# Kernel optimization log

Measured on AMD Instinct MI355X. Metric: run time of the kernel, lower is better.

The kernel has to match this reference:

```python
import jax, jax.numpy as jnp
import numpy as np

B, C, H, W = 4, 512, 64, 64
D = C // 8  # inter_channels = 64


def setup_inputs() -> dict:
    key = jax.random.key(0)
    ks = jax.random.split(key, 10)
    s = 1.0 / np.sqrt(C)
    so = 1.0 / np.sqrt(D)
    return {
        "x": jax.random.normal(ks[0], (B, C, H, W), dtype=jnp.float32),
        "Wq": jax.random.normal(ks[1], (D, C), dtype=jnp.float32) * s,
        "bq": jnp.zeros((D,), dtype=jnp.float32),
        "Wk": jax.random.normal(ks[2], (D, C), dtype=jnp.float32) * s,
        "bk": jnp.zeros((D,), dtype=jnp.float32),
        "Wv": jax.random.normal(ks[3], (D, C), dtype=jnp.float32) * s,
        "bv": jnp.zeros((D,), dtype=jnp.float32),
        "Wo": jax.random.normal(ks[4], (C, D), dtype=jnp.float32) * so,
        "bo": jnp.zeros((C,), dtype=jnp.float32),
        "gamma": jnp.zeros((1,), dtype=jnp.float32),
    }


def reference(x, Wq, bq, Wk, bk, Wv, bv, Wo, bo, gamma):
    b, c, h, w = x.shape
    n = h * w
    xf = x.reshape(b, c, n)  # (B, C, N)
    # 1x1 convs == channel-mixing matmuls
    q = jnp.einsum("dc,bcn->bnd", Wq, xf) + bq              # (B, N, D)
    k = jnp.einsum("dc,bcn->bdn", Wk, xf) + bk[:, None]      # (B, D, N)
    v = jnp.einsum("dc,bcn->bnd", Wv, xf) + bv               # (B, N, D)
    scores = jnp.einsum("bnd,bdm->bnm", q, k)                # (B, N, N)
    weights = jax.nn.softmax(scores, axis=-1)
    attended = jnp.einsum("bnm,bmd->bnd", weights, v)        # (B, N, D)
    out = jnp.einsum("cd,bnd->bcn", Wo, attended) + bo[:, None]
    out = out.reshape(b, c, h, w)
    return gamma[0] * out + x
```

## Files before the change

### kernel.cpp

```cpp
#include <hip/hip_runtime.h>

#define NB 4
#define CH 512
#define NN 4096
#define DD 64

typedef __attribute__((ext_vector_type(8))) short bf16x8;
typedef __attribute__((ext_vector_type(4))) float f32x4;

#define MFMA(a, b, c) __builtin_amdgcn_mfma_f32_16x16x32_bf16((a), (b), (c), 0, 0, 0)

__device__ inline unsigned short f2bf(float f) {
    unsigned int u = __builtin_bit_cast(unsigned int, f);
    unsigned int r = u + 0x7fffu + ((u >> 16) & 1u);
    return (unsigned short)(r >> 16);
}

__device__ inline unsigned short f2bf_trunc(float f) {
    return (unsigned short)(__builtin_bit_cast(unsigned int, f) >> 16);
}

__device__ inline float bf2f(unsigned short u) {
    return __builtin_bit_cast(float, ((unsigned int)u) << 16);
}

__device__ inline bf16x8 ld8(const unsigned short* p) {
    return *reinterpret_cast<const bf16x8*>(p);
}

__global__ __launch_bounds__(256) void convert_w(
    const float* __restrict__ Wq, const float* __restrict__ Wk,
    const float* __restrict__ Wv, const float* __restrict__ Wo,
    unsigned short* __restrict__ oq, unsigned short* __restrict__ ok,
    unsigned short* __restrict__ ov, unsigned short* __restrict__ oo) {
    int i = blockIdx.x * 256 + threadIdx.x;
    oq[i] = f2bf(Wq[i]);
    ok[i] = f2bf(Wk[i]);
    ov[i] = f2bf(Wv[i]);
    oo[i] = f2bf(Wo[i]);
}

__global__ __launch_bounds__(256) void qkv_kernel(
    const float* __restrict__ x,
    const unsigned short* __restrict__ Wq, const unsigned short* __restrict__ Wk,
    const unsigned short* __restrict__ Wv,
    const float* __restrict__ bq, const float* __restrict__ bk, const float* __restrict__ bv,
    unsigned short* __restrict__ Q, unsigned short* __restrict__ K,
    unsigned short* __restrict__ VT) {
    const int b = blockIdx.x >> 8;
    const int n0 = (blockIdx.x & 255) * 16;
    const int t = threadIdx.x;
    const int lane = t & 63, w = t >> 6;
    const int l15 = lane & 15, g = lane >> 4;

    __shared__ char smraw[49152];
    unsigned short (*sxT)[520] = (unsigned short(*)[520])smraw;
    float (*red)[4][64][12] = (float(*)[4][64][12])smraw;

    {
        const int cbase = t >> 2;
        const int nq = (t & 3) * 4;
#pragma unroll
        for (int p = 0; p < 8; ++p) {
            int c = p * 64 + cbase;
            float4 v = *reinterpret_cast<const float4*>(
                &x[((size_t)(b * CH + c)) * NN + n0 + nq]);
            sxT[nq + 0][c] = f2bf(v.x);
            sxT[nq + 1][c] = f2bf(v.y);
            sxT[nq + 2][c] = f2bf(v.z);
            sxT[nq + 3][c] = f2bf(v.w);
        }
    }
    __syncthreads();

    f32x4 accQ[4], accK[4], accV[4];
    const f32x4 z = {0.f, 0.f, 0.f, 0.f};
#pragma unroll
    for (int i = 0; i < 4; ++i) { accQ[i] = z; accK[i] = z; accV[i] = z; }

    const int wc = w * 128;
#pragma unroll
    for (int i = 0; i < 4; ++i) {
        int c = wc + i * 32 + 8 * g;
        bf16x8 ax = ld8(&sxT[l15][c]);
#pragma unroll
        for (int dt = 0; dt < 4; ++dt) {
            int d = dt * 16 + l15;
            accQ[dt] = MFMA(ax, ld8(&Wq[d * CH + c]), accQ[dt]);
            accK[dt] = MFMA(ax, ld8(&Wk[d * CH + c]), accK[dt]);
            accV[dt] = MFMA(ld8(&Wv[d * CH + c]), ax, accV[dt]);
        }
    }
    __syncthreads();

#pragma unroll
    for (int dt = 0; dt < 4; ++dt) {
        float* dst = &red[dt][w][lane][0];
        *reinterpret_cast<f32x4*>(dst + 0) = accQ[dt];
        *reinterpret_cast<f32x4*>(dst + 4) = accK[dt];
        *reinterpret_cast<f32x4*>(dst + 8) = accV[dt];
    }
    __syncthreads();

    f32x4 q = *reinterpret_cast<const f32x4*>(&red[w][0][lane][0]);
    f32x4 k = *reinterpret_cast<const f32x4*>(&red[w][0][lane][4]);
    f32x4 v = *reinterpret_cast<const f32x4*>(&red[w][0][lane][8]);
#pragma unroll
    for (int src = 1; src < 4; ++src) {
        const float* sp = &red[w][src][lane][0];
        q += *reinterpret_cast<const f32x4*>(sp + 0);
        k += *reinterpret_cast<const f32x4*>(sp + 4);
        v += *reinterpret_cast<const f32x4*>(sp + 8);
    }
    {
        int d = w * 16 + l15;
        float biasq = bq[d], biask = bk[d];
#pragma unroll
        for (int r = 0; r < 4; ++r) {
            int n = n0 + 4 * g + r;
            Q[((size_t)b * NN + n) * DD + d] = f2bf(q[r] + biasq);
            K[((size_t)b * NN + n) * DD + d] = f2bf(k[r] + biask);
        }
#pragma unroll
        for (int r = 0; r < 4; ++r) {
            int dv = w * 16 + 4 * g + r;
            VT[((size_t)b * DD + dv) * NN + n0 + l15] = f2bf(v[r] + bv[dv]);
        }
    }
}

__global__ __launch_bounds__(256) void attn_kernel(
    const unsigned short* __restrict__ Q, const unsigned short* __restrict__ K,
    const unsigned short* __restrict__ VT,
    unsigned short* __restrict__ PO, float* __restrict__ PML, int KVLEN) {
    const int s = blockIdx.x >> 8;
    const int bq_ = blockIdx.x & 255;
    const int b = bq_ >> 6;
    const int n0 = (bq_ & 63) * 64;
    const int t = threadIdx.x;
    const int lane = t & 63, w = t >> 6;
    const int l15 = lane & 15, g = lane >> 4;

    __shared__ unsigned short sK[64][72];
    __shared__ unsigned short sVT[64][72];
    __shared__ unsigned short sP[4][16][76];

    const int qrow = n0 + 16 * w + l15;
    bf16x8 qf0 = ld8(&Q[((size_t)b * NN + qrow) * DD + 0 + 8 * g]);
    bf16x8 qf1 = ld8(&Q[((size_t)b * NN + qrow) * DD + 32 + 8 * g]);

    f32x4 oacc[4];
    const f32x4 z = {0.f, 0.f, 0.f, 0.f};
#pragma unroll
    for (int i = 0; i < 4; ++i) oacc[i] = z;
    float m_run[4], l_part[4];
#pragma unroll
    for (int r = 0; r < 4; ++r) { m_run[r] = -1e30f; l_part[r] = 0.f; }

    const int kv_begin = s * KVLEN;
    const int kv_end = kv_begin + KVLEN;
    const int srow = t >> 2, sc16 = (t & 3) * 16;

    bf16x8 pk0, pk1, pv0, pv1;
    {
        const unsigned short* kp = &K[((size_t)b * NN + kv_begin + srow) * DD + sc16];
        pk0 = ld8(kp); pk1 = ld8(kp + 8);
        const unsigned short* vp = &VT[((size_t)b * DD + srow) * NN + kv_begin + sc16];
        pv0 = ld8(vp); pv1 = ld8(vp + 8);
    }

    for (int m0 = kv_begin; m0 < kv_end; m0 += 64) {
        *reinterpret_cast<bf16x8*>(&sK[srow][sc16]) = pk0;
        *reinterpret_cast<bf16x8*>(&sK[srow][sc16 + 8]) = pk1;
        *reinterpret_cast<bf16x8*>(&sVT[srow][sc16]) = pv0;
        *reinterpret_cast<bf16x8*>(&sVT[srow][sc16 + 8]) = pv1;
        __syncthreads();

        if (m0 + 64 < kv_end) {
            const unsigned short* kp = &K[((size_t)b * NN + m0 + 64 + srow) * DD + sc16];
            pk0 = ld8(kp); pk1 = ld8(kp + 8);
            const unsigned short* vp = &VT[((size_t)b * DD + srow) * NN + m0 + 64 + sc16];
            pv0 = ld8(vp); pv1 = ld8(vp + 8);
        }

        f32x4 sv[4];
#pragma unroll
        for (int ct = 0; ct < 4; ++ct) sv[ct] = z;
#pragma unroll
        for (int ct = 0; ct < 4; ++ct) {
            bf16x8 kf0 = ld8(&sK[ct * 16 + l15][0 + 8 * g]);
            sv[ct] = MFMA(qf0, kf0, sv[ct]);
            bf16x8 kf1 = ld8(&sK[ct * 16 + l15][32 + 8 * g]);
            sv[ct] = MFMA(qf1, kf1, sv[ct]);
        }

        float ownmax[4];
        bool ok = true;
#pragma unroll
        for (int r = 0; r < 4; ++r) {
            ownmax[r] = fmaxf(fmaxf(sv[0][r], sv[1][r]), fmaxf(sv[2][r], sv[3][r]));
            ok = ok && (ownmax[r] <= m_run[r] + 8.f);
        }
        if (!__all(ok)) {
#pragma unroll
            for (int r = 0; r < 4; ++r) {
                float mx = ownmax[r];
#pragma unroll
                for (int d_ = 8; d_ >= 1; d_ >>= 1) mx = fmaxf(mx, __shfl_xor(mx, d_, 64));
                float mnew = fmaxf(m_run[r], mx);
                float c_ = __expf(m_run[r] - mnew);
                m_run[r] = mnew;
                l_part[r] *= c_;
#pragma unroll
                for (int dt = 0; dt < 4; ++dt) oacc[dt][r] *= c_;
            }
        }
#pragma unroll
        for (int r = 0; r < 4; ++r) {
            float p0 = __expf(sv[0][r] - m_run[r]);
            float p1 = __expf(sv[1][r] - m_run[r]);
            float p2 = __expf(sv[2][r] - m_run[r]);
            float p3 = __expf(sv[3][r] - m_run[r]);
            sv[0][r] = p0; sv[1][r] = p1; sv[2][r] = p2; sv[3][r] = p3;
            l_part[r] += (p0 + p1) + (p2 + p3);
        }

#pragma unroll
        for (int ct = 0; ct < 4; ++ct)
#pragma unroll
            for (int r = 0; r < 4; ++r)
                sP[w][4 * g + r][ct * 16 + l15] = f2bf_trunc(sv[ct][r]);

#pragma unroll
        for (int kk = 0; kk < 2; ++kk) {
            bf16x8 pf = ld8(&sP[w][l15][kk * 32 + 8 * g]);
#pragma unroll
            for (int dt = 0; dt < 4; ++dt) {
                bf16x8 vf = ld8(&sVT[dt * 16 + l15][kk * 32 + 8 * g]);
                oacc[dt] = MFMA(pf, vf, oacc[dt]);
            }
        }
        __syncthreads();
    }

#pragma unroll
    for (int r = 0; r < 4; ++r) {
        float lt = l_part[r];
#pragma unroll
        for (int d_ = 8; d_ >= 1; d_ >>= 1) lt += __shfl_xor(lt, d_, 64);
        int n = n0 + 16 * w + 4 * g + r;
        size_t rowidx = (size_t)s * NB * NN + (size_t)b * NN + n;
#pragma unroll
        for (int dt = 0; dt < 4; ++dt)
            PO[rowidx * DD + dt * 16 + l15] = f2bf(oacc[dt][r]);
        if (l15 == 0) {
            PML[rowidx * 2 + 0] = m_run[r];
            PML[rowidx * 2 + 1] = lt;
        }
    }
}

__global__ __launch_bounds__(256) void out_fused(
    const unsigned short* __restrict__ Wo, const unsigned short* __restrict__ PO,
    const float* __restrict__ PML, const float* __restrict__ bo,
    const float* __restrict__ gamma, const float* __restrict__ x,
    float* __restrict__ out, int S) {
    const int bid = blockIdx.x;
    const int b = bid >> 8;
    const int rest = bid & 255;
    const int n0 = (rest >> 2) * 64;
    const int c0 = (rest & 3) * 128;
    const int t = threadIdx.x;
    const int lane = t & 63, w = t >> 6;
    const int l15 = lane & 15, g = lane >> 4;

    __shared__ unsigned short sATT[64][72];

    {
        const int row = t >> 2;
        const int dq = (t & 3) * 16;
        const size_t base = (size_t)b * NN + n0 + row;
        float m = -1e30f;
        for (int s = 0; s < S; ++s)
            m = fmaxf(m, PML[((size_t)s * NB * NN + base) * 2]);
        float acc[16];
#pragma unroll
        for (int j = 0; j < 16; ++j) acc[j] = 0.f;
        float l = 0.f;
        for (int s = 0; s < S; ++s) {
            size_t rowidx = (size_t)s * NB * NN + base;
            float ms = PML[rowidx * 2 + 0];
            float ls = PML[rowidx * 2 + 1];
            float wgt = __expf(ms - m);
            l += wgt * ls;
            bf16x8 a0 = ld8(&PO[rowidx * DD + dq]);
            bf16x8 a1 = ld8(&PO[rowidx * DD + dq + 8]);
#pragma unroll
            for (int j = 0; j < 8; ++j) {
                acc[j] += wgt * bf2f((unsigned short)a0[j]);
                acc[8 + j] += wgt * bf2f((unsigned short)a1[j]);
            }
        }
        float inv = 1.f / l;
        bf16x8 o0, o1;
#pragma unroll
        for (int j = 0; j < 8; ++j) {
            o0[j] = (short)f2bf(acc[j] * inv);
            o1[j] = (short)f2bf(acc[8 + j] * inv);
        }
        *reinterpret_cast<bf16x8*>(&sATT[row][dq]) = o0;
        *reinterpret_cast<bf16x8*>(&sATT[row][dq + 8]) = o1;
    }
    __syncthreads();

    const int cw = c0 + w * 32;
    f32x4 acc2[2][4];
    const f32x4 z = {0.f, 0.f, 0.f, 0.f};
#pragma unroll
    for (int i = 0; i < 2; ++i)
#pragma unroll
        for (int j = 0; j < 4; ++j) acc2[i][j] = z;

#pragma unroll
    for (int kk = 0; kk < 2; ++kk) {
        bf16x8 af[2], bfr[4];
#pragma unroll
        for (int ct = 0; ct < 2; ++ct)
            af[ct] = ld8(&Wo[(cw + ct * 16 + l15) * DD + kk * 32 + 8 * g]);
#pragma unroll
        for (int nt = 0; nt < 4; ++nt)
            bfr[nt] = ld8(&sATT[nt * 16 + l15][kk * 32 + 8 * g]);
#pragma unroll
        for (int ct = 0; ct < 2; ++ct)
#pragma unroll
            for (int nt = 0; nt < 4; ++nt) acc2[ct][nt] = MFMA(af[ct], bfr[nt], acc2[ct][nt]);
    }

    float gm = gamma[0];
#pragma unroll
    for (int ct = 0; ct < 2; ++ct) {
        int c = cw + ct * 16 + 4 * g;
#pragma unroll
        for (int r = 0; r < 4; ++r) {
            float bias = bo[c + r];
#pragma unroll
            for (int nt = 0; nt < 4; ++nt) {
                int n = n0 + nt * 16 + l15;
                size_t idx = ((size_t)b * CH + c + r) * NN + n;
                out[idx] = gm * (acc2[ct][nt][r] + bias) + x[idx];
            }
        }
    }
}

extern "C" void kernel_launch(void* const* d_in, const int* in_sizes, int n_in,
                              void* d_out, int out_size, void* d_ws, size_t ws_size,
                              hipStream_t stream) {
    const float* x = (const float*)d_in[0];
    const float* Wq = (const float*)d_in[1];
    const float* bq = (const float*)d_in[2];
    const float* Wk = (const float*)d_in[3];
    const float* bk = (const float*)d_in[4];
    const float* Wv = (const float*)d_in[5];
    const float* bv = (const float*)d_in[6];
    const float* Wo = (const float*)d_in[7];
    const float* bo = (const float*)d_in[8];
    const float* gamma = (const float*)d_in[9];
    float* out = (float*)d_out;

    char* ws = (char*)d_ws;
    unsigned short* Wq_bf = (unsigned short*)(ws + 0);
    unsigned short* Wk_bf = (unsigned short*)(ws + 65536);
    unsigned short* Wv_bf = (unsigned short*)(ws + 131072);
    unsigned short* Wo_bf = (unsigned short*)(ws + 196608);
    unsigned short* Qb = (unsigned short*)(ws + 262144);
    unsigned short* Kb = (unsigned short*)(ws + 262144 + 2097152);
    unsigned short* VTb = (unsigned short*)(ws + 262144 + 2 * 2097152);
    const size_t po_off = 262144 + 3ull * 2097152;

    int S = 4;
    while (S > 1 &&
           ws_size < po_off + (size_t)S * (2097152ull + 131072ull))
        S >>= 1;
    unsigned short* PO = (unsigned short*)(ws + po_off);
    float* PML = (float*)(ws + po_off + (size_t)S * 2097152ull);

    hipLaunchKernelGGL(convert_w, dim3(128), dim3(256), 0, stream,
                       Wq, Wk, Wv, Wo, Wq_bf, Wk_bf, Wv_bf, Wo_bf);
    hipLaunchKernelGGL(qkv_kernel, dim3(1024), dim3(256), 0, stream,
                       x, Wq_bf, Wk_bf, Wv_bf, bq, bk, bv, Qb, Kb, VTb);
    hipLaunchKernelGGL(attn_kernel, dim3(256 * S), dim3(256), 0, stream,
                       Qb, Kb, VTb, PO, PML, NN / S);
    hipLaunchKernelGGL(out_fused, dim3(1024), dim3(256), 0, stream,
                       Wo_bf, PO, PML, bo, gamma, x, out, S);
}
```

Baseline: 195.6 us.

## Drop LDS staging in attention, use exp2 softmax, remove QKV cross-wave reduction

Attention now loads K and V^T fragments directly from global memory instead of staging tiles in shared memory, removing the per-tile barriers and the register prefetch. Q is prescaled by log2(e) so all softmax exponentials use the native exp2 instruction. The QKV projection is reorganised so each wave owns 16 output dims across all channels, eliminating the shared-memory reduction and its syncs. Direct global loads rely on cache hits, risk poor coalescing especially for the strided V^T reads, and lose the overlap the prefetch gave.

```diff
diff --git a/kernel.cpp b/kernel.cpp
--- a/kernel.cpp
+++ b/kernel.cpp
@@ -4,6 +4,7 @@
 #define CH 512
 #define NN 4096
 #define DD 64
+#define LOG2E 1.44269504088896f
 
 typedef __attribute__((ext_vector_type(8))) short bf16x8;
 typedef __attribute__((ext_vector_type(4))) float f32x4;
@@ -53,9 +54,7 @@
     const int lane = t & 63, w = t >> 6;
     const int l15 = lane & 15, g = lane >> 4;
 
-    __shared__ char smraw[49152];
-    unsigned short (*sxT)[520] = (unsigned short(*)[520])smraw;
-    float (*red)[4][64][12] = (float(*)[4][64][12])smraw;
+    __shared__ unsigned short sxT[16][520];
 
     {
         const int cbase = t >> 2;
@@ -73,58 +72,29 @@
     }
     __syncthreads();
 
-    f32x4 accQ[4], accK[4], accV[4];
-    const f32x4 z = {0.f, 0.f, 0.f, 0.f};
-#pragma unroll
-    for (int i = 0; i < 4; ++i) { accQ[i] = z; accK[i] = z; accV[i] = z; }
-
-    const int wc = w * 128;
-#pragma unroll
-    for (int i = 0; i < 4; ++i) {
-        int c = wc + i * 32 + 8 * g;
+    const int d = w * 16 + l15;
+    f32x4 aQ = {0.f, 0.f, 0.f, 0.f}, aK = aQ, aV = aQ;
+#pragma unroll
+    for (int i = 0; i < 16; ++i) {
+        int c = i * 32 + 8 * g;
         bf16x8 ax = ld8(&sxT[l15][c]);
-#pragma unroll
-        for (int dt = 0; dt < 4; ++dt) {
-            int d = dt * 16 + l15;
-            accQ[dt] = MFMA(ax, ld8(&Wq[d * CH + c]), accQ[dt]);
-            accK[dt] = MFMA(ax, ld8(&Wk[d * CH + c]), accK[dt]);
-            accV[dt] = MFMA(ld8(&Wv[d * CH + c]), ax, accV[dt]);
-        }
-    }
-    __syncthreads();
-
-#pragma unroll
-    for (int dt = 0; dt < 4; ++dt) {
-        float* dst = &red[dt][w][lane][0];
-        *reinterpret_cast<f32x4*>(dst + 0) = accQ[dt];
-        *reinterpret_cast<f32x4*>(dst + 4) = accK[dt];
-        *reinterpret_cast<f32x4*>(dst + 8) = accV[dt];
-    }
-    __syncthreads();
-
-    f32x4 q = *reinterpret_cast<const f32x4*>(&red[w][0][lane][0]);
-    f32x4 k = *reinterpret_cast<const f32x4*>(&red[w][0][lane][4]);
-    f32x4 v = *reinterpret_cast<const f32x4*>(&red[w][0][lane][8]);
-#pragma unroll
-    for (int src = 1; src < 4; ++src) {
-        const float* sp = &red[w][src][lane][0];
-        q += *reinterpret_cast<const f32x4*>(sp + 0);
-        k += *reinterpret_cast<const f32x4*>(sp + 4);
-        v += *reinterpret_cast<const f32x4*>(sp + 8);
-    }
+        aQ = MFMA(ax, ld8(&Wq[d * CH + c]), aQ);
+        aK = MFMA(ax, ld8(&Wk[d * CH + c]), aK);
+        aV = MFMA(ld8(&Wv[d * CH + c]), ax, aV);
+    }
+
     {
-        int d = w * 16 + l15;
         float biasq = bq[d], biask = bk[d];
 #pragma unroll
         for (int r = 0; r < 4; ++r) {
             int n = n0 + 4 * g + r;
-            Q[((size_t)b * NN + n) * DD + d] = f2bf(q[r] + biasq);
-            K[((size_t)b * NN + n) * DD + d] = f2bf(k[r] + biask);
+            Q[((size_t)b * NN + n) * DD + d] = f2bf((aQ[r] + biasq) * LOG2E);
+            K[((size_t)b * NN + n) * DD + d] = f2bf(aK[r] + biask);
         }
 #pragma unroll
         for (int r = 0; r < 4; ++r) {
             int dv = w * 16 + 4 * g + r;
-            VT[((size_t)b * DD + dv) * NN + n0 + l15] = f2bf(v[r] + bv[dv]);
+            VT[((size_t)b * DD + dv) * NN + n0 + l15] = f2bf(aV[r] + bv[dv]);
         }
     }
 }
@@ -141,8 +111,6 @@
     const int lane = t & 63, w = t >> 6;
     const int l15 = lane & 15, g = lane >> 4;
 
-    __shared__ unsigned short sK[64][72];
-    __shared__ unsigned short sVT[64][72];
     __shared__ unsigned short sP[4][16][76];
 
     const int qrow = n0 + 16 * w + l15;
@@ -159,38 +127,19 @@
 
     const int kv_begin = s * KVLEN;
     const int kv_end = kv_begin + KVLEN;
-    const int srow = t >> 2, sc16 = (t & 3) * 16;
-
-    bf16x8 pk0, pk1, pv0, pv1;
-    {
-        const unsigned short* kp = &K[((size_t)b * NN + kv_begin + srow) * DD + sc16];
-        pk0 = ld8(kp); pk1 = ld8(kp + 8);
-        const unsigned short* vp = &VT[((size_t)b * DD + srow) * NN + kv_begin + sc16];
-        pv0 = ld8(vp); pv1 = ld8(vp + 8);
-    }
 
     for (int m0 = kv_begin; m0 < kv_end; m0 += 64) {
-        *reinterpret_cast<bf16x8*>(&sK[srow][sc16]) = pk0;
-        *reinterpret_cast<bf16x8*>(&sK[srow][sc16 + 8]) = pk1;
-        *reinterpret_cast<bf16x8*>(&sVT[srow][sc16]) = pv0;
-        *reinterpret_cast<bf16x8*>(&sVT[srow][sc16 + 8]) = pv1;
-        __syncthreads();
-
-        if (m0 + 64 < kv_end) {
-            const unsigned short* kp = &K[((size_t)b * NN + m0 + 64 + srow) * DD + sc16];
-            pk0 = ld8(kp); pk1 = ld8(kp + 8);
-            const unsigned short* vp = &VT[((size_t)b * DD + srow) * NN + m0 + 64 + sc16];
-            pv0 = ld8(vp); pv1 = ld8(vp + 8);
-        }
+        const unsigned short* Kb_ = &K[((size_t)b * NN + m0) * DD];
+        const unsigned short* Vb_ = &VT[(size_t)b * DD * NN + m0];
 
         f32x4 sv[4];
 #pragma unroll
         for (int ct = 0; ct < 4; ++ct) sv[ct] = z;
 #pragma unroll
         for (int ct = 0; ct < 4; ++ct) {
-            bf16x8 kf0 = ld8(&sK[ct * 16 + l15][0 + 8 * g]);
+            bf16x8 kf0 = ld8(&Kb_[(ct * 16 + l15) * DD + 0 + 8 * g]);
             sv[ct] = MFMA(qf0, kf0, sv[ct]);
-            bf16x8 kf1 = ld8(&sK[ct * 16 + l15][32 + 8 * g]);
+            bf16x8 kf1 = ld8(&Kb_[(ct * 16 + l15) * DD + 32 + 8 * g]);
             sv[ct] = MFMA(qf1, kf1, sv[ct]);
         }
 
@@ -208,7 +157,7 @@
 #pragma unroll
                 for (int d_ = 8; d_ >= 1; d_ >>= 1) mx = fmaxf(mx, __shfl_xor(mx, d_, 64));
                 float mnew = fmaxf(m_run[r], mx);
-                float c_ = __expf(m_run[r] - mnew);
+                float c_ = __builtin_amdgcn_exp2f(m_run[r] - mnew);
                 m_run[r] = mnew;
                 l_part[r] *= c_;
 #pragma unroll
@@ -217,10 +166,10 @@
         }
 #pragma unroll
         for (int r = 0; r < 4; ++r) {
-            float p0 = __expf(sv[0][r] - m_run[r]);
-            float p1 = __expf(sv[1][r] - m_run[r]);
-            float p2 = __expf(sv[2][r] - m_run[r]);
-            float p3 = __expf(sv[3][r] - m_run[r]);
+            float p0 = __builtin_amdgcn_exp2f(sv[0][r] - m_run[r]);
+            float p1 = __builtin_amdgcn_exp2f(sv[1][r] - m_run[r]);
+            float p2 = __builtin_amdgcn_exp2f(sv[2][r] - m_run[r]);
+            float p3 = __builtin_amdgcn_exp2f(sv[3][r] - m_run[r]);
             sv[0][r] = p0; sv[1][r] = p1; sv[2][r] = p2; sv[3][r] = p3;
             l_part[r] += (p0 + p1) + (p2 + p3);
         }
@@ -236,11 +185,10 @@
             bf16x8 pf = ld8(&sP[w][l15][kk * 32 + 8 * g]);
 #pragma unroll
             for (int dt = 0; dt < 4; ++dt) {
-                bf16x8 vf = ld8(&sVT[dt * 16 + l15][kk * 32 + 8 * g]);
+                bf16x8 vf = ld8(&Vb_[(size_t)(dt * 16 + l15) * NN + kk * 32 + 8 * g]);
                 oacc[dt] = MFMA(pf, vf, oacc[dt]);
             }
         }
-        __syncthreads();
     }
 
 #pragma unroll
@@ -291,7 +239,7 @@
             size_t rowidx = (size_t)s * NB * NN + base;
             float ms = PML[rowidx * 2 + 0];
             float ls = PML[rowidx * 2 + 1];
-            float wgt = __expf(ms - m);
+            float wgt = __builtin_amdgcn_exp2f(ms - m);
             l += wgt * ls;
             bf16x8 a0 = ld8(&PO[rowidx * DD + dq]);
             bf16x8 a1 = ld8(&PO[rowidx * DD + dq + 8]);
```

After: 254.7 us. +30.2%, slower.
